# Optimization experiments

Hardware: AMD Instinct MI355X
Metric: run time of the kernel (lower is better)

## Reference

```python
import jax, jax.numpy as jnp
import numpy as np

# Dimensions
T, B = 128, 512
NTOK, NINP, NHID = 512, 512, 600
NB, BS, TOPK = 6, 100, 4          # num_blocks, block_size = nhid//num_blocks, update_topk
H, DK, DV, ATT = 4, 64, 85, 340   # input-attention heads, key dim, value dim (H*DV == attention_out)
H2, DK2, DV2 = 4, 32, 32          # communication (step) attention dims


def setup_inputs() -> dict:
    key = jax.random.key(0)
    ks = jax.random.split(key, 16)
    def rn(k, shape, s=0.05):
        return (jax.random.normal(k, shape) * s).astype(jnp.float32)
    return dict(
        input=jax.random.normal(ks[0], (T, B, NTOK), dtype=jnp.float32),
        h0=jnp.zeros((B, NHID), jnp.float32),
        masks=jnp.ones((T, B, 1), jnp.float32),
        enc_W=rn(ks[1], (NTOK, NINP)), enc_b=jnp.zeros((NINP,), jnp.float32),
        Wq_in=rn(ks[2], (BS, H * DK)), Wk_in=rn(ks[3], (NINP, H * DK)), Wv_in=rn(ks[4], (NINP, H * DV)),
        W_ih=rn(ks[5], (NB, ATT, 3 * BS)), W_hh=rn(ks[6], (NB, BS, 3 * BS)),
        b_ih=jnp.zeros((NB, 3 * BS), jnp.float32), b_hh=jnp.zeros((NB, 3 * BS), jnp.float32),
        Wq_c=rn(ks[7], (BS, H2 * DK2)), Wk_c=rn(ks[8], (BS, H2 * DK2)),
        Wv_c=rn(ks[9], (BS, H2 * DV2)), Wo_c=rn(ks[10], (H2 * DV2, BS)),
        dec_W=rn(ks[11], (NHID, NTOK)), dec_b=jnp.zeros((NTOK,), jnp.float32),
    )


def _rim_scan(emb, masks, h0, Wq_in, Wk_in, Wv_in, W_ih, W_hh, b_ih, b_hh,
              Wq_c, Wk_c, Wv_c, Wo_c):
    inv_sdk = 1.0 / np.sqrt(DK).astype(np.float32)
    inv_sdk2 = 1.0 / np.sqrt(DK2).astype(np.float32)

    def step(h, xm):
        xt, mt = xm                      # [B,NINP], [B,1]
        h = h * mt                       # episode-reset gating
        hb = h.reshape(B, NB, BS)
        # --- input attention over {real input, null} slots ---
        slots = jnp.stack([xt, jnp.zeros_like(xt)], axis=1)          # [B,2,NINP]
        k = (slots @ Wk_in).reshape(B, 2, H, DK)
        v = (slots @ Wv_in).reshape(B, 2, H, DV)
        q = (hb @ Wq_in).reshape(B, NB, H, DK)
        att = jax.nn.softmax(jnp.einsum('bnhd,bshd->bnhs', q, k) * inv_sdk, axis=-1)
        act = 1.0 - att[..., 1].mean(-1)                             # [B,NB] attention to real input
        kth = jax.lax.top_k(act, TOPK)[0][:, -1:]
        mask = (act >= kth).astype(h.dtype)                          # [B,NB] top-k block activation
        inp_use = jnp.einsum('bnhs,bshd->bnhd', att, v).reshape(B, NB, ATT)
        # --- block-diagonal GRU update ---
        gi = jnp.einsum('bnd,nde->bne', inp_use, W_ih) + b_ih
        gh = jnp.einsum('bnd,nde->bne', hb, W_hh) + b_hh
        gi_r, gi_z, gi_n = jnp.split(gi, 3, axis=-1)
        gh_r, gh_z, gh_n = jnp.split(gh, 3, axis=-1)
        r = jax.nn.sigmoid(gi_r + gh_r)
        z = jax.nn.sigmoid(gi_z + gh_z)
        n = jnp.tanh(gi_n + r * gh_n)
        hn = (1.0 - z) * n + z * hb
        # --- step (communication) attention across blocks, residual ---
        qc = (hn @ Wq_c).reshape(B, NB, H2, DK2)
        kc = (hn @ Wk_c).reshape(B, NB, H2, DK2)
        vc = (hn @ Wv_c).reshape(B, NB, H2, DV2)
        ac = jax.nn.softmax(jnp.einsum('bnhd,bmhd->bhnm', qc, kc) * inv_sdk2, axis=-1)
        co = jnp.einsum('bhnm,bmhd->bnhd', ac, vc).reshape(B, NB, H2 * DV2) @ Wo_c
        hc = hn + co
        # --- only top-k active blocks are updated ---
        m = mask[..., None]
        hf = (m * hc + (1.0 - m) * hb).reshape(B, NHID)
        return hf, (hf, mask)

    h_last, (hs, bmask) = jax.lax.scan(step, h0, (emb, masks))
    return hs, h_last, bmask


def reference(input, h0, masks, enc_W, enc_b, Wq_in, Wk_in, Wv_in,
              W_ih, W_hh, b_ih, b_hh, Wq_c, Wk_c, Wv_c, Wo_c, dec_W, dec_b):
    emb = input @ enc_W + enc_b                                      # encoder Linear [T,B,NINP]
    hs, h_last, bmask = _rim_scan(emb, masks, h0, Wq_in, Wk_in, Wv_in,
                                  W_ih, W_hh, b_ih, b_hh, Wq_c, Wk_c, Wv_c, Wo_c)
    dec = hs @ dec_W + dec_b                                         # decoder [T,B,NTOK]
    return dec
```

## Files before the change

### kernel.cpp

```cpp
#include <hip/hip_runtime.h>
#include <math.h>

#define T_STEPS 128
#define BATCH   512
#define NTOK    512
#define NINP    512
#define NHID    600
#define NBK     6
#define BS      100
#define HH      4
#define DK      64
#define DV      85
#define ATT     340
#define H2      4
#define DK2     32
#define DV2     32
#define G3      300
#define VN      340
#define KAPN    400
#define CN      740
#define CNP     768
#define UN2     1800
#define UN2P    1920
#define UK0     128
#define KV0     512
#define DECKP   640
#define SW      2

typedef __attribute__((ext_vector_type(8))) short short8;
typedef __attribute__((ext_vector_type(4))) float f32x4;

__device__ __forceinline__ float sigf(float x) { return 1.f / (1.f + expf(-x)); }
__device__ __forceinline__ unsigned short f2b(float f) {
    unsigned u = __float_as_uint(f);
    unsigned r = (u + 0x7fffu + ((u >> 16) & 1u)) >> 16;
    return (unsigned short)r;
}
__device__ __forceinline__ float b2f(unsigned short u) {
    return __uint_as_float(((unsigned)u) << 16);
}
__device__ __forceinline__ void split3(float x, unsigned short& hi,
                                       unsigned short& mid, unsigned short& lo) {
    hi = f2b(x);
    float r1 = x - b2f(hi);
    mid = f2b(r1);
    lo = f2b(r1 - b2f(mid));
}

struct ZOff { int div; long s1; long s2; };
__device__ __forceinline__ long zoff(ZOff z, int bz) {
    return (long)(bz / z.div) * z.s1 + (long)(bz % z.div) * z.s2;
}

__global__ __launch_bounds__(256) void gemm6(
    const unsigned short* __restrict__ A, long aZ, int aZdiv,
    const unsigned short* __restrict__ B, long bZ,
    float* __restrict__ C, long cZ, int ldc, int Nreal,
    const float* __restrict__ bias, int K0)
{
    const int bz = blockIdx.z;
    A += (long)(bz / aZdiv) * aZ;
    B += (long)bz * bZ;
    C += (long)bz * cZ;
    const int LDA = 3 * K0;
    const int m0 = blockIdx.y * 128, n0 = blockIdx.x * 128;
    __shared__ __align__(16) unsigned short As[128 * 64];
    __shared__ __align__(16) unsigned short Bs[128 * 64];
    const int tid = threadIdx.x;
    const int lane = tid & 63;
    const int wid = tid >> 6;
    const int wr = wid >> 1, wc = wid & 1;

    f32x4 acc[4][4];
#pragma unroll
    for (int m = 0; m < 4; m++)
#pragma unroll
        for (int n = 0; n < 4; n++)
#pragma unroll
            for (int v = 0; v < 4; v++) acc[m][n][v] = 0.f;

    const int segA[6] = {0, 0, 1, 0, 2, 1};
    const int segB[6] = {0, 1, 0, 2, 0, 1};
    for (int p = 0; p < 6; p++) {
        const unsigned short* Ap = A + segA[p] * K0;
        const unsigned short* Bp = B + segB[p] * K0;
        for (int k0 = 0; k0 < K0; k0 += 64) {
            short8 ra[4], rb[4];
#pragma unroll
            for (int q = 0; q < 4; q++) {
                int idx = (q << 8) + tid;
                int r = idx >> 3, ce = (idx & 7) << 3;
                ra[q] = *(const short8*)&Ap[(long)(m0 + r) * LDA + k0 + ce];
                rb[q] = *(const short8*)&Bp[(long)(n0 + r) * LDA + k0 + ce];
            }
            __syncthreads();
#pragma unroll
            for (int q = 0; q < 4; q++) {
                int idx = (q << 8) + tid;
                int r = idx >> 3, ce = (idx & 7) << 3;
                *(short8*)&As[r * 64 + ce] = ra[q];
                *(short8*)&Bs[r * 64 + ce] = rb[q];
            }
            __syncthreads();
#pragma unroll
            for (int kk = 0; kk < 2; kk++) {
                short8 af[4], bfr[4];
#pragma unroll
                for (int m = 0; m < 4; m++)
                    af[m] = *(const short8*)&As[(wr * 64 + m * 16 + (lane & 15)) * 64 + kk * 32 + (lane >> 4) * 8];
#pragma unroll
                for (int n = 0; n < 4; n++)
                    bfr[n] = *(const short8*)&Bs[(wc * 64 + n * 16 + (lane & 15)) * 64 + kk * 32 + (lane >> 4) * 8];
#pragma unroll
                for (int m = 0; m < 4; m++)
#pragma unroll
                    for (int n = 0; n < 4; n++)
                        acc[m][n] = __builtin_amdgcn_mfma_f32_16x16x32_bf16(af[m], bfr[n], acc[m][n], 0, 0, 0);
            }
        }
    }
#pragma unroll
    for (int m = 0; m < 4; m++) {
        int rbase = m0 + wr * 64 + m * 16 + (lane >> 4) * 4;
#pragma unroll
        for (int n = 0; n < 4; n++) {
            int col = n0 + wc * 64 + n * 16 + (lane & 15);
            if (col < Nreal) {
                float bv = bias ? bias[col] : 0.f;
#pragma unroll
                for (int v = 0; v < 4; v++)
                    C[(long)(rbase + v) * ldc + col] = acc[m][n][v] + bv;
            }
        }
    }
}

__global__ __launch_bounds__(256) void gemm6_kv(
    const unsigned short* __restrict__ A,
    const unsigned short* __restrict__ B,
    unsigned short* __restrict__ A_U,
    float* __restrict__ Kbuf,
    const float* __restrict__ bias, int K0, int MU)
{
    const int LDA = 3 * K0;
    const int m0 = blockIdx.y * 128, n0 = blockIdx.x * 128;
    __shared__ __align__(16) unsigned short As[128 * 64];
    __shared__ __align__(16) unsigned short Bs[128 * 64];
    const int tid = threadIdx.x;
    const int lane = tid & 63;
    const int wid = tid >> 6;
    const int wr = wid >> 1, wc = wid & 1;

    f32x4 acc[4][4];
#pragma unroll
    for (int m = 0; m < 4; m++)
#pragma unroll
        for (int n = 0; n < 4; n++)
#pragma unroll
            for (int v = 0; v < 4; v++) acc[m][n][v] = 0.f;

    const int segA[6] = {0, 0, 1, 0, 2, 1};
    const int segB[6] = {0, 1, 0, 2, 0, 1};
    for (int p = 0; p < 6; p++) {
        const unsigned short* Ap = A + segA[p] * K0;
        const unsigned short* Bp = B + segB[p] * K0;
        for (int k0 = 0; k0 < K0; k0 += 64) {
            short8 ra[4], rb[4];
#pragma unroll
            for (int q = 0; q < 4; q++) {
                int idx = (q << 8) + tid;
                int r = idx >> 3, ce = (idx & 7) << 3;
                ra[q] = *(const short8*)&Ap[(long)(m0 + r) * LDA + k0 + ce];
                rb[q] = *(const short8*)&Bp[(long)(n0 + r) * LDA + k0 + ce];
            }
            __syncthreads();
#pragma unroll
            for (int q = 0; q < 4; q++) {
                int idx = (q << 8) + tid;
                int r = idx >> 3, ce = (idx & 7) << 3;
                *(short8*)&As[r * 64 + ce] = ra[q];
                *(short8*)&Bs[r * 64 + ce] = rb[q];
            }
            __syncthreads();
#pragma unroll
            for (int kk = 0; kk < 2; kk++) {
                short8 af[4], bfr[4];
#pragma unroll
                for (int m = 0; m < 4; m++)
                    af[m] = *(const short8*)&As[(wr * 64 + m * 16 + (lane & 15)) * 64 + kk * 32 + (lane >> 4) * 8];
#pragma unroll
                for (int n = 0; n < 4; n++)
                    bfr[n] = *(const short8*)&Bs[(wc * 64 + n * 16 + (lane & 15)) * 64 + kk * 32 + (lane >> 4) * 8];
#pragma unroll
                for (int m = 0; m < 4; m++)
#pragma unroll
                    for (int n = 0; n < 4; n++)
                        acc[m][n] = __builtin_amdgcn_mfma_f32_16x16x32_bf16(af[m], bfr[n], acc[m][n], 0, 0, 0);
            }
        }
    }
#pragma unroll
    for (int m = 0; m < 4; m++) {
        int rbase = m0 + wr * 64 + m * 16 + (lane >> 4) * 4;
#pragma unroll
        for (int n = 0; n < 4; n++) {
            int col = n0 + wc * 64 + n * 16 + (lane & 15);
            if (col < CN) {
                float bv = bias[col];
                if (col < VN) {
                    int h = col / DV, kk2 = col - h * DV;
#pragma unroll
                    for (int v = 0; v < 4; v++) {
                        float val = acc[m][n][v] + bv;
                        unsigned short hi, mid, lo;
                        split3(val, hi, mid, lo);
                        long base = ((long)h * MU + (rbase + v)) * (3 * UK0) + kk2;
                        A_U[base] = hi;
                        A_U[base + UK0] = mid;
                        A_U[base + 2 * UK0] = lo;
                    }
                } else {
                    int kc = col - VN;
#pragma unroll
                    for (int v = 0; v < 4; v++)
                        Kbuf[(long)(rbase + v) * KAPN + kc] = acc[m][n][v] + bv;
                }
            }
        }
    }
}

__global__ __launch_bounds__(256) void gemm_mfma(
    const unsigned short* __restrict__ A,
    const unsigned short* __restrict__ B,
    float* __restrict__ C, int ldc,
    const float* __restrict__ bias, int Kp)
{
    const int m0 = blockIdx.y * 128, n0 = blockIdx.x * 128;
    __shared__ __align__(16) unsigned short As[128 * 64];
    __shared__ __align__(16) unsigned short Bs[128 * 64];
    const int tid = threadIdx.x;
    const int lane = tid & 63;
    const int wid = tid >> 6;
    const int wr = wid >> 1, wc = wid & 1;

    f32x4 acc[4][4];
#pragma unroll
    for (int m = 0; m < 4; m++)
#pragma unroll
        for (int n = 0; n < 4; n++)
#pragma unroll
            for (int v = 0; v < 4; v++) acc[m][n][v] = 0.f;

    for (int k0 = 0; k0 < Kp; k0 += 64) {
        short8 ra[4], rb[4];
#pragma unroll
        for (int q = 0; q < 4; q++) {
            int idx = (q << 8) + tid;
            int r = idx >> 3, ce = (idx & 7) << 3;
            ra[q] = *(const short8*)&A[(long)(m0 + r) * Kp + k0 + ce];
            rb[q] = *(const short8*)&B[(long)(n0 + r) * Kp + k0 + ce];
        }
        __syncthreads();
#pragma unroll
        for (int q = 0; q < 4; q++) {
            int idx = (q << 8) + tid;
            int r = idx >> 3, ce = (idx & 7) << 3;
            *(short8*)&As[r * 64 + ce] = ra[q];
            *(short8*)&Bs[r * 64 + ce] = rb[q];
        }
        __syncthreads();
#pragma unroll
        for (int kk = 0; kk < 2; kk++) {
            short8 af[4], bfr[4];
#pragma unroll
            for (int m = 0; m < 4; m++)
                af[m] = *(const short8*)&As[(wr * 64 + m * 16 + (lane & 15)) * 64 + kk * 32 + (lane >> 4) * 8];
#pragma unroll
            for (int n = 0; n < 4; n++)
                bfr[n] = *(const short8*)&Bs[(wc * 64 + n * 16 + (lane & 15)) * 64 + kk * 32 + (lane >> 4) * 8];
#pragma unroll
            for (int m = 0; m < 4; m++)
#pragma unroll
                for (int n = 0; n < 4; n++)
                    acc[m][n] = __builtin_amdgcn_mfma_f32_16x16x32_bf16(af[m], bfr[n], acc[m][n], 0, 0, 0);
        }
    }
#pragma unroll
    for (int m = 0; m < 4; m++) {
        int rbase = m0 + wr * 64 + m * 16 + (lane >> 4) * 4;
#pragma unroll
        for (int n = 0; n < 4; n++) {
            int col = n0 + wc * 64 + n * 16 + (lane & 15);
            float bv = bias ? bias[col] : 0.f;
#pragma unroll
            for (int v = 0; v < 4; v++)
                C[(long)(rbase + v) * ldc + col] = acc[m][n][v] + bv;
        }
    }
}

__global__ __launch_bounds__(256) void sgemm(
    const float* __restrict__ A, ZOff za, int lda,
    const float* __restrict__ B, ZOff zb, int ldb,
    float* __restrict__ C, ZOff zc, int ldc,
    int M, int N, int K)
{
    const int bz = blockIdx.z;
    A += zoff(za, bz);
    B += zoff(zb, bz);
    C += zoff(zc, bz);
    const int m0 = blockIdx.y * 128, n0 = blockIdx.x * 64;
    __shared__ float As[16][132];
    __shared__ float Bs[16][68];
    const int tid = threadIdx.x;
    const int tm = tid >> 4, tn = tid & 15;
    const int ar = tid >> 1, ak = (tid & 1) * 8;
    const int bk = tid >> 4, bn = (tid & 15) * 4;

    float acc[8][4];
#pragma unroll
    for (int i = 0; i < 8; i++)
#pragma unroll
        for (int j = 0; j < 4; j++) acc[i][j] = 0.f;

    for (int k0 = 0; k0 < K; k0 += 16) {
        float av[8], bv[4];
#pragma unroll
        for (int j = 0; j < 8; j++) {
            int gk = k0 + ak + j;
            av[j] = (gk < K) ? A[(long)(m0 + ar) * lda + gk] : 0.f;
        }
#pragma unroll
        for (int j = 0; j < 4; j++) {
            int gk = k0 + bk, gn = n0 + bn + j;
            bv[j] = (gk < K && gn < N) ? B[(long)gk * ldb + gn] : 0.f;
        }
        __syncthreads();
#pragma unroll
        for (int j = 0; j < 8; j++) As[ak + j][ar] = av[j];
#pragma unroll
        for (int j = 0; j < 4; j++) Bs[bk][bn + j] = bv[j];
        __syncthreads();
#pragma unroll
        for (int kk = 0; kk < 16; kk++) {
            float a[8], b[4];
#pragma unroll
            for (int i = 0; i < 8; i++) a[i] = As[kk][tm * 8 + i];
#pragma unroll
            for (int j = 0; j < 4; j++) b[j] = Bs[kk][tn * 4 + j];
#pragma unroll
            for (int i = 0; i < 8; i++)
#pragma unroll
                for (int j = 0; j < 4; j++)
                    acc[i][j] += a[i] * b[j];
        }
    }
#pragma unroll
    for (int i = 0; i < 8; i++) {
        int gm = m0 + tm * 8 + i;
#pragma unroll
        for (int j = 0; j < 4; j++) {
            int gn = n0 + tn * 4 + j;
            if (gn < N) C[(long)gm * ldc + gn] = acc[i][j];
        }
    }
}

__global__ __launch_bounds__(256) void prep_wqt(const float* __restrict__ Wq_in,
                                                float* __restrict__ WqT)
{
    int idx = blockIdx.x * 256 + threadIdx.x;
    if (idx >= HH * DK * BS) return;
    int h = idx / (DK * BS), r = idx - h * DK * BS, d = r / BS, w = r - d * BS;
    WqT[idx] = Wq_in[w * (HH * DK) + h * DK + d];
}

__global__ __launch_bounds__(256) void prep_whh4(const float* __restrict__ W_hh,
                                                 float* __restrict__ Whh4)
{
    int idx = blockIdx.x * 256 + threadIdx.x;
    if (idx >= NBK * BS * G3) return;
    int n = idx / (BS * G3), r = idx - n * (BS * G3);
    int d = r / G3, e = r - d * G3;
    int g = e / BS, w = e - g * BS;
    Whh4[(((long)n * BS + d) * BS + w) * 4 + g] = W_hh[idx];
}

__global__ __launch_bounds__(256) void bias_k(const float* __restrict__ enc_b,
                                              const float* __restrict__ Wk,
                                              float* __restrict__ kbf)
{
    int j = threadIdx.x;
    if (j >= HH * DK) return;
    float acc = 0.f;
    for (int d = 0; d < NINP; d++) acc += enc_b[d] * Wk[d * (HH * DK) + j];
    kbf[j] = acc;
}

__global__ __launch_bounds__(256) void bias_c_kernel(const float* __restrict__ enc_b,
                                                     const float* __restrict__ Wv,
                                                     const float* __restrict__ kbf,
                                                     const float* __restrict__ WqT,
                                                     float* __restrict__ bias_c)
{
    int j = blockIdx.x * 256 + threadIdx.x;
    if (j >= CNP) return;
    float acc = 0.f;
    if (j < VN) {
        for (int d = 0; d < NINP; d++) acc += enc_b[d] * Wv[d * (HH * DV) + j];
    } else if (j < CN) {
        int r = j - VN;
        int h = r / BS, w = r - h * BS;
        for (int d = 0; d < DK; d++)
            acc += kbf[h * DK + d] * WqT[(h * DK + d) * BS + w];
    }
    bias_c[j] = acc;
}

__global__ __launch_bounds__(256) void cvt_dec(const float* __restrict__ dec_W,
                                               unsigned short* __restrict__ dst)
{
    int idx = blockIdx.x * 256 + threadIdx.x;
    if (idx >= NTOK * DECKP) return;
    int n = idx / DECKP, k = idx - n * DECKP;
    dst[idx] = f2b(k < NHID ? dec_W[k * NTOK + n] : 0.f);
}

__global__ __launch_bounds__(256) void cvt_split_ew(const float* __restrict__ EWfull,
                                                    unsigned short* __restrict__ dst)
{
    int idx = blockIdx.x * 256 + threadIdx.x;
    if (idx >= CNP * NTOK) return;
    int n = idx / NTOK, k = idx - n * NTOK;
    float x = (n < CN) ? EWfull[(long)k * CNP + n] : 0.f;
    unsigned short hi, mid, lo;
    split3(x, hi, mid, lo);
    long base = (long)n * (3 * KV0) + k;
    dst[base] = hi;
    dst[base + KV0] = mid;
    dst[base + 2 * KV0] = lo;
}

__global__ __launch_bounds__(256) void cvt_split_bu2(const float* __restrict__ W_ih,
                                                     unsigned short* __restrict__ dst)
{
    int idx = blockIdx.x * 256 + threadIdx.x;
    if (idx >= HH * UN2P * UK0) return;
    int h = idx / (UN2P * UK0), r = idx - h * (UN2P * UK0);
    int j = r / UK0, kk = r - j * UK0;
    float x = 0.f;
    if (kk < DV && j < UN2) {
        int n = j / G3, e = j - n * G3;
        x = W_ih[((long)n * ATT + h * DV + kk) * G3 + e];
    }
    unsigned short hi, mid, lo;
    split3(x, hi, mid, lo);
    long base = ((long)h * UN2P + j) * (3 * UK0) + kk;
    dst[base] = hi;
    dst[base + UK0] = mid;
    dst[base + 2 * UK0] = lo;
}

__global__ __launch_bounds__(256) void cvt_split_in(const float* __restrict__ src,
                                                    unsigned short* __restrict__ dst, long rows)
{
    long total = rows * NTOK;
    long i = (long)blockIdx.x * 256 + threadIdx.x;
    long stride = (long)gridDim.x * 256;
    for (; i < total; i += stride) {
        long row = i / NTOK; int k = (int)(i - row * NTOK);
        unsigned short hi, mid, lo;
        split3(src[i], hi, mid, lo);
        long base = row * (3 * KV0) + k;
        dst[base] = hi;
        dst[base + KV0] = mid;
        dst[base + 2 * KV0] = lo;
    }
}

__global__ __launch_bounds__(1024) void step_fused(
    const float* __restrict__ h_prev,
    const float* __restrict__ masks_t,
    const float* __restrict__ Kbuf,
    const float* __restrict__ U,
    const float* __restrict__ b_ih, const float* __restrict__ b_hh,
    const float* __restrict__ Whh4,
    const float* __restrict__ Wq_c, const float* __restrict__ Wk_c,
    const float* __restrict__ Wv_c, const float* __restrict__ Wo_c,
    float* __restrict__ h_out,
    unsigned short* __restrict__ A_dec,
    int s_step, int MU)
{
    const int b0 = blockIdx.x * SW, tid = threadIdx.x;
    __shared__ __align__(16) float hbT[NHID][SW];
    __shared__ __align__(16) float hnT[NHID][SW];
    __shared__ __align__(16) float kp[SW][KAPN];
    __shared__ __align__(16) float qcb[SW][768], kcb[SW][768], vcb[SW][768];
    __shared__ __align__(16) float coT[NBK * 128][SW];
    __shared__ float part[SW * 96];
    __shared__ float att[SW][24], mk[SW][NBK];
    __shared__ float lg[SW][144];

    const long rowd0 = (long)s_step * BATCH + b0;
    const int n2 = (tid < 600) ? tid / 100 : 0;
    const int w2 = (tid < 600) ? tid - n2 * 100 : 0;

    float uraw[HH][3][SW];
    if (tid < 600) {
#pragma unroll
        for (int h = 0; h < HH; h++) {
            const float* Uh = U + ((long)h * MU + rowd0) * UN2 + n2 * G3;
#pragma unroll
            for (int s = 0; s < SW; s++)
#pragma unroll
                for (int g = 0; g < 3; g++)
                    uraw[h][g][s] = Uh[(long)s * UN2 + g * BS + w2];
        }
    }

    for (int i = tid; i < SW * NHID; i += 1024) {
        int s = i / NHID, j = i - s * NHID;
        hbT[j][s] = h_prev[(long)(b0 + s) * NHID + j] * masks_t[b0 + s];
    }
    for (int i = tid; i < SW * KAPN; i += 1024) {
        int s = i / KAPN, j = i - s * KAPN;
        kp[s][j] = Kbuf[(rowd0 + s) * KAPN + j];
    }
    __syncthreads();
    if (tid < SW * 96) {
        int g = tid >> 2, q = tid & 3;
        int s = g / 24, r = g - s * 24;
        int n = r >> 2, h = r & 3;
        float acc = 0.f;
        int w0 = q * 25;
        for (int w = w0; w < w0 + 25; w++) acc += hbT[n * BS + w][s] * kp[s][h * BS + w];
        part[tid] = acc;
    }
    __syncthreads();
    if (tid < SW * 24) {
        int s = tid / 24, r = tid - s * 24;
        float l = part[tid * 4] + part[tid * 4 + 1] + part[tid * 4 + 2] + part[tid * 4 + 3];
        att[s][r] = sigf(l * 0.125f);
    }
    __syncthreads();
    if (tid < SW) {
        float a[NBK], av[NBK];
        for (int n = 0; n < NBK; n++) {
            av[n] = 0.25f * (att[tid][n * 4] + att[tid][n * 4 + 1] + att[tid][n * 4 + 2] + att[tid][n * 4 + 3]);
            a[n] = av[n];
        }
        for (int i = 0; i < 4; i++) {
            int mx = i;
            for (int j = i + 1; j < NBK; j++) if (a[j] > a[mx]) mx = j;
            float t = a[i]; a[i] = a[mx]; a[mx] = t;
        }
        float kth = a[3];
        for (int n = 0; n < NBK; n++) mk[tid][n] = (av[n] >= kth) ? 1.f : 0.f;
    }

    if (tid < 600) {
        float gi[3][SW], gh[3][SW];
#pragma unroll
        for (int g = 0; g < 3; g++) {
            float bi = b_ih[n2 * G3 + g * BS + w2];
            float bh = b_hh[n2 * G3 + g * BS + w2];
#pragma unroll
            for (int s = 0; s < SW; s++) { gi[g][s] = bi; gh[g][s] = bh; }
        }
#pragma unroll
        for (int h = 0; h < HH; h++)
#pragma unroll
            for (int s = 0; s < SW; s++) {
                float a = att[s][n2 * 4 + h];
#pragma unroll
                for (int g = 0; g < 3; g++)
                    gi[g][s] += a * uraw[h][g][s];
            }
        const f32x4* Wn4 = ((const f32x4*)Whh4) + (long)n2 * BS * BS + w2;
#pragma unroll 10
        for (int d = 0; d < BS; d++) {
            f32x4 wv = Wn4[(long)d * BS];
            float2 hv = *(const float2*)&hbT[n2 * BS + d][0];
            gh[0][0] += wv[0] * hv.x; gh[0][1] += wv[0] * hv.y;
            gh[1][0] += wv[1] * hv.x; gh[1][1] += wv[1] * hv.y;
            gh[2][0] += wv[2] * hv.x; gh[2][1] += wv[2] * hv.y;
        }
        float2 hnv;
        {
            float rr0 = sigf(gi[0][0] + gh[0][0]);
            float zz0 = sigf(gi[1][0] + gh[1][0]);
            float ng0 = tanhf(gi[2][0] + rr0 * gh[2][0]);
            hnv.x = (1.f - zz0) * ng0 + zz0 * hbT[n2 * BS + w2][0];
            float rr1 = sigf(gi[0][1] + gh[0][1]);
            float zz1 = sigf(gi[1][1] + gh[1][1]);
            float ng1 = tanhf(gi[2][1] + rr1 * gh[2][1]);
            hnv.y = (1.f - zz1) * ng1 + zz1 * hbT[n2 * BS + w2][1];
        }
        *(float2*)&hnT[n2 * BS + w2][0] = hnv;
    }
    __syncthreads();

    if (tid < 768) {
        const int mat = tid >> 8, r = tid & 255, ng = r >> 7, c = r & 127;
        const float* W = (mat == 0) ? Wq_c : ((mat == 1) ? Wk_c : Wv_c);
        float acc[3][SW];
#pragma unroll
        for (int j = 0; j < 3; j++)
#pragma unroll
            for (int s = 0; s < SW; s++) acc[j][s] = 0.f;
#pragma unroll 10
        for (int d = 0; d < BS; d++) {
            float wv = W[d * 128 + c];
#pragma unroll
            for (int j = 0; j < 3; j++) {
                float2 hv = *(const float2*)&hnT[(ng * 3 + j) * BS + d][0];
                acc[j][0] += wv * hv.x;
                acc[j][1] += wv * hv.y;
            }
        }
        float (*dst)[768] = (mat == 0) ? qcb : ((mat == 1) ? kcb : vcb);
#pragma unroll
        for (int j = 0; j < 3; j++)
#pragma unroll
            for (int s = 0; s < SW; s++)
                dst[s][(ng * 3 + j) * 128 + c] = acc[j][s];
    }
    __syncthreads();

    if (tid < SW * 144) {
        int s = tid / 144, r = tid - s * 144;
        int h = r / 36, r2 = r - h * 36, n = r2 / NBK, m = r2 - n * NBK;
        float sv = 0.f;
#pragma unroll
        for (int e4 = 0; e4 < 8; e4++) {
            f32x4 qv = *(const f32x4*)&qcb[s][n * 128 + h * 32 + e4 * 4];
            f32x4 kv = *(const f32x4*)&kcb[s][m * 128 + h * 32 + e4 * 4];
            sv += qv[0] * kv[0] + qv[1] * kv[1] + qv[2] * kv[2] + qv[3] * kv[3];
        }
        lg[s][r] = sv * 0.17677669529663687f;
    }
    __syncthreads();
    if (tid < SW * 24) {
        int s = tid / 24, r = tid - s * 24;
        float* row = &lg[s][r * NBK];
        float mx = row[0];
        for (int m = 1; m < NBK; m++) mx = fmaxf(mx, row[m]);
        float sv = 0.f;
        for (int m = 0; m < NBK; m++) { row[m] = expf(row[m] - mx); sv += row[m]; }
        float inv = 1.f / sv;
        for (int m = 0; m < NBK; m++) row[m] *= inv;
    }
    __syncthreads();
    for (int idx = tid; idx < SW * 768; idx += 1024) {
        int s = idx / 768, r = idx - s * 768;
        int n = r >> 7, d = r & 127, h = d >> 5;
        float a = 0.f;
#pragma unroll
        for (int m = 0; m < NBK; m++) a += lg[s][h * 36 + n * NBK + m] * vcb[s][m * 128 + d];
        coT[r][s] = a;
    }
    __syncthreads();

    if (tid < 600) {
        float a0 = 0.f, a1 = 0.f;
#pragma unroll 8
        for (int d = 0; d < 128; d++) {
            float wv = Wo_c[d * BS + w2];
            float2 cv = *(const float2*)&coT[n2 * 128 + d][0];
            a0 += wv * cv.x;
            a1 += wv * cv.y;
        }
        float2 res;
        float hc0 = hnT[n2 * BS + w2][0] + a0;
        float hc1 = hnT[n2 * BS + w2][1] + a1;
        res.x = (mk[0][n2] > 0.5f) ? hc0 : hbT[n2 * BS + w2][0];
        res.y = (mk[1][n2] > 0.5f) ? hc1 : hbT[n2 * BS + w2][1];
        *(float2*)&hbT[n2 * BS + w2][0] = res;
    }
    __syncthreads();
    for (int i = tid; i < SW * NHID; i += 1024) {
        int s = i / NHID, j = i - s * NHID;
        h_out[(long)(b0 + s) * NHID + j] = hbT[j][s];
    }
    for (int i = tid; i < SW * DECKP; i += 1024) {
        int s = i / DECKP, col = i - s * DECKP;
        A_dec[(rowd0 + s) * DECKP + col] = f2b(col < NHID ? hbT[col][s] : 0.f);
    }
}

extern "C" void kernel_launch(void* const* d_in, const int* in_sizes, int n_in,
                              void* d_out, int out_size, void* d_ws, size_t ws_size,
                              hipStream_t stream)
{
    const float* input = (const float*)d_in[0];
    const float* h0    = (const float*)d_in[1];
    const float* masks = (const float*)d_in[2];
    const float* enc_W = (const float*)d_in[3];
    const float* enc_b = (const float*)d_in[4];
    const float* Wq_in = (const float*)d_in[5];
    const float* Wk_in = (const float*)d_in[6];
    const float* Wv_in = (const float*)d_in[7];
    const float* W_ih  = (const float*)d_in[8];
    const float* W_hh  = (const float*)d_in[9];
    const float* b_ih  = (const float*)d_in[10];
    const float* b_hh  = (const float*)d_in[11];
    const float* Wq_c  = (const float*)d_in[12];
    const float* Wk_c  = (const float*)d_in[13];
    const float* Wv_c  = (const float*)d_in[14];
    const float* Wo_c  = (const float*)d_in[15];
    const float* dec_W = (const float*)d_in[16];
    const float* dec_b = (const float*)d_in[17];
    float* out = (float*)d_out;

    const size_t AL = 256;
    auto pad = [&](size_t x) { return (x + AL - 1) & ~(AL - 1); };
    size_t fixedB = pad((size_t)NTOK * CNP * 4)
                  + pad((size_t)NTOK * 256 * 4)
                  + pad((size_t)HH * DK * BS * 4)
                  + pad((size_t)256 * 4)
                  + pad((size_t)CNP * 4)
                  + pad((size_t)NBK * BS * BS * 4 * 4)
                  + pad((size_t)CNP * 3 * KV0 * 2)
                  + pad((size_t)HH * UN2P * 3 * UK0 * 2)
                  + pad((size_t)NTOK * DECKP * 2)
                  + 2 * pad((size_t)BATCH * NHID * 4);
    auto perC = [&](int C) {
        size_t MU = (size_t)C * BATCH;
        return pad(MU * 3 * KV0 * 2)
             + pad(MU * KAPN * 4)
             + pad((size_t)HH * MU * 3 * UK0 * 2)
             + pad((size_t)HH * MU * UN2 * 4)
             + pad(MU * DECKP * 2);
    };
    int C = 8;
    while (C > 1 && fixedB + perC(C) > ws_size) C >>= 1;
    const int MU = C * BATCH;
    const int NCH = T_STEPS / C;

    char* p = (char*)d_ws;
    auto alloc = [&](size_t bytes) { char* r = p; p += pad(bytes); return r; };
    float*          EWfull = (float*)alloc((size_t)NTOK * CNP * 4);
    float*          EWk    = (float*)alloc((size_t)NTOK * 256 * 4);
    float*          WqT    = (float*)alloc((size_t)HH * DK * BS * 4);
    float*          kbf    = (float*)alloc((size_t)256 * 4);
    float*          bias_c = (float*)alloc((size_t)CNP * 4);
    float*          Whh4   = (float*)alloc((size_t)NBK * BS * BS * 4 * 4);
    unsigned short* B_vkap = (unsigned short*)alloc((size_t)CNP * 3 * KV0 * 2);
    unsigned short* B_U    = (unsigned short*)alloc((size_t)HH * UN2P * 3 * UK0 * 2);
    unsigned short* B_dec  = (unsigned short*)alloc((size_t)NTOK * DECKP * 2);
    float*          hA     = (float*)alloc((size_t)BATCH * NHID * 4);
    float*          hB     = (float*)alloc((size_t)BATCH * NHID * 4);
    unsigned short* A_in   = (unsigned short*)alloc((size_t)MU * 3 * KV0 * 2);
    float*          Kbuf   = (float*)alloc((size_t)MU * KAPN * 4);
    unsigned short* A_U    = (unsigned short*)alloc((size_t)HH * MU * 3 * UK0 * 2);
    float*          Ubuf   = (float*)alloc((size_t)HH * MU * UN2 * 4);
    unsigned short* A_dec  = (unsigned short*)alloc((size_t)MU * DECKP * 2);

    dim3 blk(256);
    ZOff z0 = {1, 0, 0};

    sgemm<<<dim3(6, 4, 1), blk, 0, stream>>>(
        enc_W, z0, NINP, Wv_in, z0, HH * DV, EWfull, z0, CNP, NTOK, VN, NINP);
    sgemm<<<dim3(4, 4, 1), blk, 0, stream>>>(
        enc_W, z0, NINP, Wk_in, z0, HH * DK, EWk, z0, 256, NTOK, HH * DK, NINP);
    prep_wqt<<<dim3((HH * DK * BS + 255) / 256), blk, 0, stream>>>(Wq_in, WqT);
    prep_whh4<<<dim3((NBK * BS * G3 + 255) / 256), blk, 0, stream>>>(W_hh, Whh4);
    sgemm<<<dim3(2, 4, HH), blk, 0, stream>>>(
        EWk, ZOff{1, DK, 0}, 256, WqT, ZOff{1, (long)DK * BS, 0}, BS,
        EWfull + VN, ZOff{1, BS, 0}, CNP, NTOK, BS, DK);
    bias_k<<<dim3(1), blk, 0, stream>>>(enc_b, Wk_in, kbf);
    bias_c_kernel<<<dim3(3), blk, 0, stream>>>(enc_b, Wv_in, kbf, WqT, bias_c);
    cvt_split_ew<<<dim3((CNP * NTOK + 255) / 256), blk, 0, stream>>>(EWfull, B_vkap);
    cvt_split_bu2<<<dim3((HH * UN2P * UK0 + 255) / 256), blk, 0, stream>>>(W_ih, B_U);
    cvt_dec<<<dim3((NTOK * DECKP + 255) / 256), blk, 0, stream>>>(dec_W, B_dec);

    const float* hp = h0;
    float* hbufs[2] = { hA, hB };
    int t = 0;
    for (int c = 0; c < NCH; c++) {
        cvt_split_in<<<dim3(2048), blk, 0, stream>>>(
            input + (size_t)c * MU * NTOK, A_in, MU);
        gemm6_kv<<<dim3(CNP / 128, MU / 128, 1), blk, 0, stream>>>(
            A_in, B_vkap, A_U, Kbuf, bias_c, KV0, MU);
        gemm6<<<dim3(UN2P / 128, MU / 128, HH), blk, 0, stream>>>(
            A_U, (long)MU * 3 * UK0, 1, B_U, (long)UN2P * 3 * UK0,
            Ubuf, (long)MU * UN2, UN2, UN2, nullptr, UK0);
        for (int s = 0; s < C; s++, t++) {
            float* hout = hbufs[t & 1];
            step_fused<<<dim3(BATCH / SW), dim3(1024), 0, stream>>>(
                hp, masks + (size_t)t * BATCH, Kbuf, Ubuf, b_ih, b_hh, Whh4,
                Wq_c, Wk_c, Wv_c, Wo_c, hout, A_dec, s, MU);
            hp = hout;
        }
        gemm_mfma<<<dim3(NTOK / 128, MU / 128, 1), blk, 0, stream>>>(
            A_dec, B_dec, out + (size_t)c * MU * NTOK, NTOK, dec_b, DECKP);
    }
}
```

Before: 6.374 ms.

## Fuse per-step recurrent kernels into one chunk kernel; stage GEMM tiles via global_load_lds

```diff
diff --git a/kernel.cpp b/kernel.cpp
--- a/kernel.cpp
+++ b/kernel.cpp
@@ -30,6 +30,9 @@
 typedef __attribute__((ext_vector_type(8))) short short8;
 typedef __attribute__((ext_vector_type(4))) float f32x4;
 
+typedef __attribute__((address_space(1))) const unsigned int* g1ptr;
+typedef __attribute__((address_space(3))) unsigned int* l3ptr;
+
 __device__ __forceinline__ float sigf(float x) { return 1.f / (1.f + expf(-x)); }
 __device__ __forceinline__ unsigned short f2b(float f) {
     unsigned u = __float_as_uint(f);
@@ -50,6 +53,21 @@
 struct ZOff { int div; long s1; long s2; };
 __device__ __forceinline__ long zoff(ZOff z, int bz) {
     return (long)(bz / z.div) * z.s1 + (long)(bz % z.div) * z.s2;
+}
+
+__device__ __forceinline__ void stage_tile(const unsigned short* __restrict__ gbase,
+                                           long rowStride, int m0, int k0,
+                                           unsigned short* lds, int tid)
+{
+    const int w = tid >> 6;
+#pragma unroll
+    for (int q = 0; q < 4; q++) {
+        int idx = (q << 8) + tid;
+        int r = idx >> 3, ce = (idx & 7) << 3;
+        const unsigned short* g = gbase + (long)(m0 + r) * rowStride + k0 + ce;
+        unsigned short* l = lds + q * 2048 + w * 512;
+        __builtin_amdgcn_global_load_lds((g1ptr)(const void*)g, (l3ptr)(void*)l, 16, 0, 0);
+    }
 }
 
 __global__ __launch_bounds__(256) void gemm6(
@@ -85,22 +103,9 @@
         const unsigned short* Ap = A + segA[p] * K0;
         const unsigned short* Bp = B + segB[p] * K0;
         for (int k0 = 0; k0 < K0; k0 += 64) {
-            short8 ra[4], rb[4];
-#pragma unroll
-            for (int q = 0; q < 4; q++) {
-                int idx = (q << 8) + tid;
-                int r = idx >> 3, ce = (idx & 7) << 3;
-                ra[q] = *(const short8*)&Ap[(long)(m0 + r) * LDA + k0 + ce];
-                rb[q] = *(const short8*)&Bp[(long)(n0 + r) * LDA + k0 + ce];
-            }
             __syncthreads();
-#pragma unroll
-            for (int q = 0; q < 4; q++) {
-                int idx = (q << 8) + tid;
-                int r = idx >> 3, ce = (idx & 7) << 3;
-                *(short8*)&As[r * 64 + ce] = ra[q];
-                *(short8*)&Bs[r * 64 + ce] = rb[q];
-            }
+            stage_tile(Ap, LDA, m0, k0, As, tid);
+            stage_tile(Bp, LDA, n0, k0, Bs, tid);
             __syncthreads();
 #pragma unroll
             for (int kk = 0; kk < 2; kk++) {
@@ -165,22 +170,9 @@
         const unsigned short* Ap = A + segA[p] * K0;
         const unsigned short* Bp = B + segB[p] * K0;
         for (int k0 = 0; k0 < K0; k0 += 64) {
-            short8 ra[4], rb[4];
-#pragma unroll
-            for (int q = 0; q < 4; q++) {
-                int idx = (q << 8) + tid;
-                int r = idx >> 3, ce = (idx & 7) << 3;
-                ra[q] = *(const short8*)&Ap[(long)(m0 + r) * LDA + k0 + ce];
-                rb[q] = *(const short8*)&Bp[(long)(n0 + r) * LDA + k0 + ce];
-            }
             __syncthreads();
-#pragma unroll
-            for (int q = 0; q < 4; q++) {
-                int idx = (q << 8) + tid;
-                int r = idx >> 3, ce = (idx & 7) << 3;
-                *(short8*)&As[r * 64 + ce] = ra[q];
-                *(short8*)&Bs[r * 64 + ce] = rb[q];
-            }
+            stage_tile(Ap, LDA, m0, k0, As, tid);
+            stage_tile(Bp, LDA, n0, k0, Bs, tid);
             __syncthreads();
 #pragma unroll
             for (int kk = 0; kk < 2; kk++) {
@@ -253,22 +245,9 @@
             for (int v = 0; v < 4; v++) acc[m][n][v] = 0.f;
 
     for (int k0 = 0; k0 < Kp; k0 += 64) {
-        short8 ra[4], rb[4];
-#pragma unroll
-        for (int q = 0; q < 4; q++) {
-            int idx = (q << 8) + tid;
-            int r = idx >> 3, ce = (idx & 7) << 3;
-            ra[q] = *(const short8*)&A[(long)(m0 + r) * Kp + k0 + ce];
-            rb[q] = *(const short8*)&B[(long)(n0 + r) * Kp + k0 + ce];
-        }
-        __syncthreads();
-#pragma unroll
-        for (int q = 0; q < 4; q++) {
-            int idx = (q << 8) + tid;
-            int r = idx >> 3, ce = (idx & 7) << 3;
-            *(short8*)&As[r * 64 + ce] = ra[q];
-            *(short8*)&Bs[r * 64 + ce] = rb[q];
-        }
+        __syncthreads();
+        stage_tile(A, Kp, m0, k0, As, tid);
+        stage_tile(B, Kp, n0, k0, Bs, tid);
         __syncthreads();
 #pragma unroll
         for (int kk = 0; kk < 2; kk++) {
@@ -479,18 +458,18 @@
     }
 }
 
-__global__ __launch_bounds__(1024) void step_fused(
-    const float* __restrict__ h_prev,
-    const float* __restrict__ masks_t,
+__global__ __launch_bounds__(1024) void step_chunk(
+    const float* __restrict__ h_in,
+    const float* __restrict__ masks_c,
     const float* __restrict__ Kbuf,
     const float* __restrict__ U,
     const float* __restrict__ b_ih, const float* __restrict__ b_hh,
     const float* __restrict__ Whh4,
     const float* __restrict__ Wq_c, const float* __restrict__ Wk_c,
     const float* __restrict__ Wv_c, const float* __restrict__ Wo_c,
-    float* __restrict__ h_out,
+    float* __restrict__ h_outG,
     unsigned short* __restrict__ A_dec,
-    int s_step, int MU)
+    int nsteps, int MU)
 {
     const int b0 = blockIdx.x * SW, tid = threadIdx.x;
     __shared__ __align__(16) float hbT[NHID][SW];
@@ -502,190 +481,198 @@
     __shared__ float att[SW][24], mk[SW][NBK];
     __shared__ float lg[SW][144];
 
-    const long rowd0 = (long)s_step * BATCH + b0;
     const int n2 = (tid < 600) ? tid / 100 : 0;
     const int w2 = (tid < 600) ? tid - n2 * 100 : 0;
 
-    float uraw[HH][3][SW];
-    if (tid < 600) {
-#pragma unroll
-        for (int h = 0; h < HH; h++) {
-            const float* Uh = U + ((long)h * MU + rowd0) * UN2 + n2 * G3;
-#pragma unroll
-            for (int s = 0; s < SW; s++)
-#pragma unroll
-                for (int g = 0; g < 3; g++)
-                    uraw[h][g][s] = Uh[(long)s * UN2 + g * BS + w2];
-        }
-    }
-
     for (int i = tid; i < SW * NHID; i += 1024) {
         int s = i / NHID, j = i - s * NHID;
-        hbT[j][s] = h_prev[(long)(b0 + s) * NHID + j] * masks_t[b0 + s];
-    }
-    for (int i = tid; i < SW * KAPN; i += 1024) {
-        int s = i / KAPN, j = i - s * KAPN;
-        kp[s][j] = Kbuf[(rowd0 + s) * KAPN + j];
-    }
-    __syncthreads();
-    if (tid < SW * 96) {
-        int g = tid >> 2, q = tid & 3;
-        int s = g / 24, r = g - s * 24;
-        int n = r >> 2, h = r & 3;
-        float acc = 0.f;
-        int w0 = q * 25;
-        for (int w = w0; w < w0 + 25; w++) acc += hbT[n * BS + w][s] * kp[s][h * BS + w];
-        part[tid] = acc;
-    }
-    __syncthreads();
-    if (tid < SW * 24) {
-        int s = tid / 24, r = tid - s * 24;
-        float l = part[tid * 4] + part[tid * 4 + 1] + part[tid * 4 + 2] + part[tid * 4 + 3];
-        att[s][r] = sigf(l * 0.125f);
-    }
-    __syncthreads();
-    if (tid < SW) {
-        float a[NBK], av[NBK];
-        for (int n = 0; n < NBK; n++) {
-            av[n] = 0.25f * (att[tid][n * 4] + att[tid][n * 4 + 1] + att[tid][n * 4 + 2] + att[tid][n * 4 + 3]);
-            a[n] = av[n];
-        }
-        for (int i = 0; i < 4; i++) {
-            int mx = i;
-            for (int j = i + 1; j < NBK; j++) if (a[j] > a[mx]) mx = j;
-            float t = a[i]; a[i] = a[mx]; a[mx] = t;
-        }
-        float kth = a[3];
-        for (int n = 0; n < NBK; n++) mk[tid][n] = (av[n] >= kth) ? 1.f : 0.f;
-    }
-
-    if (tid < 600) {
-        float gi[3][SW], gh[3][SW];
-#pragma unroll
-        for (int g = 0; g < 3; g++) {
-            float bi = b_ih[n2 * G3 + g * BS + w2];
-            float bh = b_hh[n2 * G3 + g * BS + w2];
-#pragma unroll
-            for (int s = 0; s < SW; s++) { gi[g][s] = bi; gh[g][s] = bh; }
-        }
-#pragma unroll
-        for (int h = 0; h < HH; h++)
-#pragma unroll
-            for (int s = 0; s < SW; s++) {
-                float a = att[s][n2 * 4 + h];
-#pragma unroll
-                for (int g = 0; g < 3; g++)
-                    gi[g][s] += a * uraw[h][g][s];
-            }
-        const f32x4* Wn4 = ((const f32x4*)Whh4) + (long)n2 * BS * BS + w2;
+        hbT[j][s] = h_in[(long)(b0 + s) * NHID + j];
+    }
+
+    for (int st = 0; st < nsteps; st++) {
+        const long rowd0 = (long)st * BATCH + b0;
+
+        float uraw[HH][3][SW];
+        if (tid < 600) {
+#pragma unroll
+            for (int h = 0; h < HH; h++) {
+                const float* Uh = U + ((long)h * MU + rowd0) * UN2 + n2 * G3;
+#pragma unroll
+                for (int s = 0; s < SW; s++)
+#pragma unroll
+                    for (int g = 0; g < 3; g++)
+                        uraw[h][g][s] = Uh[(long)s * UN2 + g * BS + w2];
+            }
+        }
+        __syncthreads();
+        for (int i = tid; i < SW * NHID; i += 1024) {
+            int s = i / NHID, j = i - s * NHID;
+            hbT[j][s] *= masks_c[rowd0 + s];
+        }
+        for (int i = tid; i < SW * KAPN; i += 1024) {
+            int s = i / KAPN, j = i - s * KAPN;
+            kp[s][j] = Kbuf[(rowd0 + s) * KAPN + j];
+        }
+        __syncthreads();
+        if (tid < SW * 96) {
+            int g = tid >> 2, q = tid & 3;
+            int s = g / 24, r = g - s * 24;
+            int n = r >> 2, h = r & 3;
+            float acc = 0.f;
+            int w0 = q * 25;
+            for (int w = w0; w < w0 + 25; w++) acc += hbT[n * BS + w][s] * kp[s][h * BS + w];
+            part[tid] = acc;
+        }
+        __syncthreads();
+        if (tid < SW * 24) {
+            int s = tid / 24, r = tid - s * 24;
+            float l = part[tid * 4] + part[tid * 4 + 1] + part[tid * 4 + 2] + part[tid * 4 + 3];
+            att[s][r] = sigf(l * 0.125f);
+        }
+        __syncthreads();
+        if (tid < SW) {
+            float a[NBK], av[NBK];
+            for (int n = 0; n < NBK; n++) {
+                av[n] = 0.25f * (att[tid][n * 4] + att[tid][n * 4 + 1] + att[tid][n * 4 + 2] + att[tid][n * 4 + 3]);
+                a[n] = av[n];
+            }
+            for (int i = 0; i < 4; i++) {
+                int mx = i;
+                for (int j = i + 1; j < NBK; j++) if (a[j] > a[mx]) mx = j;
+                float t = a[i]; a[i] = a[mx]; a[mx] = t;
+            }
+            float kth = a[3];
+            for (int n = 0; n < NBK; n++) mk[tid][n] = (av[n] >= kth) ? 1.f : 0.f;
+        }
+
+        if (tid < 600) {
+            float gi[3][SW], gh[3][SW];
+#pragma unroll
+            for (int g = 0; g < 3; g++) {
+                float bi = b_ih[n2 * G3 + g * BS + w2];
+                float bh = b_hh[n2 * G3 + g * BS + w2];
+#pragma unroll
+                for (int s = 0; s < SW; s++) { gi[g][s] = bi; gh[g][s] = bh; }
+            }
+#pragma unroll
+            for (int h = 0; h < HH; h++)
+#pragma unroll
+                for (int s = 0; s < SW; s++) {
+                    float a = att[s][n2 * 4 + h];
+#pragma unroll
+                    for (int g = 0; g < 3; g++)
+                        gi[g][s] += a * uraw[h][g][s];
+                }
+            const f32x4* Wn4 = ((const f32x4*)Whh4) + (long)n2 * BS * BS + w2;
 #pragma unroll 10
-        for (int d = 0; d < BS; d++) {
-            f32x4 wv = Wn4[(long)d * BS];
-            float2 hv = *(const float2*)&hbT[n2 * BS + d][0];
-            gh[0][0] += wv[0] * hv.x; gh[0][1] += wv[0] * hv.y;
-            gh[1][0] += wv[1] * hv.x; gh[1][1] += wv[1] * hv.y;
-            gh[2][0] += wv[2] * hv.x; gh[2][1] += wv[2] * hv.y;
-        }
-        float2 hnv;
-        {
-            float rr0 = sigf(gi[0][0] + gh[0][0]);
-            float zz0 = sigf(gi[1][0] + gh[1][0]);
-            float ng0 = tanhf(gi[2][0] + rr0 * gh[2][0]);
-            hnv.x = (1.f - zz0) * ng0 + zz0 * hbT[n2 * BS + w2][0];
-            float rr1 = sigf(gi[0][1] + gh[0][1]);
-            float zz1 = sigf(gi[1][1] + gh[1][1]);
-            float ng1 = tanhf(gi[2][1] + rr1 * gh[2][1]);
-            hnv.y = (1.f - zz1) * ng1 + zz1 * hbT[n2 * BS + w2][1];
-        }
-        *(float2*)&hnT[n2 * BS + w2][0] = hnv;
-    }
-    __syncthreads();
-
-    if (tid < 768) {
-        const int mat = tid >> 8, r = tid & 255, ng = r >> 7, c = r & 127;
-        const float* W = (mat == 0) ? Wq_c : ((mat == 1) ? Wk_c : Wv_c);
-        float acc[3][SW];
-#pragma unroll
-        for (int j = 0; j < 3; j++)
-#pragma unroll
-            for (int s = 0; s < SW; s++) acc[j][s] = 0.f;
+            for (int d = 0; d < BS; d++) {
+                f32x4 wv = Wn4[(long)d * BS];
+                float2 hv = *(const float2*)&hbT[n2 * BS + d][0];
+                gh[0][0] += wv[0] * hv.x; gh[0][1] += wv[0] * hv.y;
+                gh[1][0] += wv[1] * hv.x; gh[1][1] += wv[1] * hv.y;
+                gh[2][0] += wv[2] * hv.x; gh[2][1] += wv[2] * hv.y;
+            }
+            float2 hnv;
+            {
+                float rr0 = sigf(gi[0][0] + gh[0][0]);
+                float zz0 = sigf(gi[1][0] + gh[1][0]);
+                float ng0 = tanhf(gi[2][0] + rr0 * gh[2][0]);
+                hnv.x = (1.f - zz0) * ng0 + zz0 * hbT[n2 * BS + w2][0];
+                float rr1 = sigf(gi[0][1] + gh[0][1]);
+                float zz1 = sigf(gi[1][1] + gh[1][1]);
+                float ng1 = tanhf(gi[2][1] + rr1 * gh[2][1]);
+                hnv.y = (1.f - zz1) * ng1 + zz1 * hbT[n2 * BS + w2][1];
+            }
+            *(float2*)&hnT[n2 * BS + w2][0] = hnv;
+        }
+        __syncthreads();
+
+        if (tid < 768) {
+            const int mat = tid >> 8, r = tid & 255, ng = r >> 7, c = r & 127;
+            const float* W = (mat == 0) ? Wq_c : ((mat == 1) ? Wk_c : Wv_c);
+            float acc[3][SW];
+#pragma unroll
+            for (int j = 0; j < 3; j++)
+#pragma unroll
+                for (int s = 0; s < SW; s++) acc[j][s] = 0.f;
 #pragma unroll 10
-        for (int d = 0; d < BS; d++) {
-            float wv = W[d * 128 + c];
-#pragma unroll
-            for (int j = 0; j < 3; j++) {
-                float2 hv = *(const float2*)&hnT[(ng * 3 + j) * BS + d][0];
-                acc[j][0] += wv * hv.x;
-                acc[j][1] += wv * hv.y;
-            }
-        }
-        float (*dst)[768] = (mat == 0) ? qcb : ((mat == 1) ? kcb : vcb);
-#pragma unroll
-        for (int j = 0; j < 3; j++)
-#pragma unroll
-            for (int s = 0; s < SW; s++)
-                dst[s][(ng * 3 + j) * 128 + c] = acc[j][s];
-    }
-    __syncthreads();
-
-    if (tid < SW * 144) {
-        int s = tid / 144, r = tid - s * 144;
-        int h = r / 36, r2 = r - h * 36, n = r2 / NBK, m = r2 - n * NBK;
-        float sv = 0.f;
-#pragma unroll
-        for (int e4 = 0; e4 < 8; e4++) {
-            f32x4 qv = *(const f32x4*)&qcb[s][n * 128 + h * 32 + e4 * 4];
-            f32x4 kv = *(const f32x4*)&kcb[s][m * 128 + h * 32 + e4 * 4];
-            sv += qv[0] * kv[0] + qv[1] * kv[1] + qv[2] * kv[2] + qv[3] * kv[3];
-        }
-        lg[s][r] = sv * 0.17677669529663687f;
-    }
-    __syncthreads();
-    if (tid < SW * 24) {
-        int s = tid / 24, r = tid - s * 24;
-        float* row = &lg[s][r * NBK];
-        float mx = row[0];
-        for (int m = 1; m < NBK; m++) mx = fmaxf(mx, row[m]);
-        float sv = 0.f;
-        for (int m = 0; m < NBK; m++) { row[m] = expf(row[m] - mx); sv += row[m]; }
-        float inv = 1.f / sv;
-        for (int m = 0; m < NBK; m++) row[m] *= inv;
-    }
-    __syncthreads();
-    for (int idx = tid; idx < SW * 768; idx += 1024) {
-        int s = idx / 768, r = idx - s * 768;
-        int n = r >> 7, d = r & 127, h = d >> 5;
-        float a = 0.f;
-#pragma unroll
-        for (int m = 0; m < NBK; m++) a += lg[s][h * 36 + n * NBK + m] * vcb[s][m * 128 + d];
-        coT[r][s] = a;
-    }
-    __syncthreads();
-
-    if (tid < 600) {
-        float a0 = 0.f, a1 = 0.f;
+            for (int d = 0; d < BS; d++) {
+                float wv = W[d * 128 + c];
+#pragma unroll
+                for (int j = 0; j < 3; j++) {
+                    float2 hv = *(const float2*)&hnT[(ng * 3 + j) * BS + d][0];
+                    acc[j][0] += wv * hv.x;
+                    acc[j][1] += wv * hv.y;
+                }
+            }
+            float (*dst)[768] = (mat == 0) ? qcb : ((mat == 1) ? kcb : vcb);
+#pragma unroll
+            for (int j = 0; j < 3; j++)
+#pragma unroll
+                for (int s = 0; s < SW; s++)
+                    dst[s][(ng * 3 + j) * 128 + c] = acc[j][s];
+        }
+        __syncthreads();
+
+        if (tid < SW * 144) {
+            int s = tid / 144, r = tid - s * 144;
+            int h = r / 36, r2 = r - h * 36, n = r2 / NBK, m = r2 - n * NBK;
+            float sv = 0.f;
+#pragma unroll
+            for (int e4 = 0; e4 < 8; e4++) {
+                f32x4 qv = *(const f32x4*)&qcb[s][n * 128 + h * 32 + e4 * 4];
+                f32x4 kv = *(const f32x4*)&kcb[s][m * 128 + h * 32 + e4 * 4];
+                sv += qv[0] * kv[0] + qv[1] * kv[1] + qv[2] * kv[2] + qv[3] * kv[3];
+            }
+            lg[s][r] = sv * 0.17677669529663687f;
+        }
+        __syncthreads();
+        if (tid < SW * 24) {
+            int s = tid / 24, r = tid - s * 24;
+            float* row = &lg[s][r * NBK];
+            float mx = row[0];
+            for (int m = 1; m < NBK; m++) mx = fmaxf(mx, row[m]);
+            float sv = 0.f;
+            for (int m = 0; m < NBK; m++) { row[m] = expf(row[m] - mx); sv += row[m]; }
+            float inv = 1.f / sv;
+            for (int m = 0; m < NBK; m++) row[m] *= inv;
+        }
+        __syncthreads();
+        for (int idx = tid; idx < SW * 768; idx += 1024) {
+            int s = idx / 768, r = idx - s * 768;
+            int n = r >> 7, d = r & 127, h = d >> 5;
+            float a = 0.f;
+#pragma unroll
+            for (int m = 0; m < NBK; m++) a += lg[s][h * 36 + n * NBK + m] * vcb[s][m * 128 + d];
+            coT[r][s] = a;
+        }
+        __syncthreads();
+
+        if (tid < 600) {
+            float a0 = 0.f, a1 = 0.f;
 #pragma unroll 8
-        for (int d = 0; d < 128; d++) {
-            float wv = Wo_c[d * BS + w2];
-            float2 cv = *(const float2*)&coT[n2 * 128 + d][0];
-            a0 += wv * cv.x;
-            a1 += wv * cv.y;
-        }
-        float2 res;
-        float hc0 = hnT[n2 * BS + w2][0] + a0;
-        float hc1 = hnT[n2 * BS + w2][1] + a1;
-        res.x = (mk[0][n2] > 0.5f) ? hc0 : hbT[n2 * BS + w2][0];
-        res.y = (mk[1][n2] > 0.5f) ? hc1 : hbT[n2 * BS + w2][1];
-        *(float2*)&hbT[n2 * BS + w2][0] = res;
-    }
-    __syncthreads();
+            for (int d = 0; d < 128; d++) {
+                float wv = Wo_c[d * BS + w2];
+                float2 cv = *(const float2*)&coT[n2 * 128 + d][0];
+                a0 += wv * cv.x;
+                a1 += wv * cv.y;
+            }
+            float2 res;
+            float hc0 = hnT[n2 * BS + w2][0] + a0;
+            float hc1 = hnT[n2 * BS + w2][1] + a1;
+            res.x = (mk[0][n2] > 0.5f) ? hc0 : hbT[n2 * BS + w2][0];
+            res.y = (mk[1][n2] > 0.5f) ? hc1 : hbT[n2 * BS + w2][1];
+            *(float2*)&hbT[n2 * BS + w2][0] = res;
+        }
+        __syncthreads();
+        for (int i = tid; i < SW * DECKP; i += 1024) {
+            int s = i / DECKP, col = i - s * DECKP;
+            A_dec[(rowd0 + s) * DECKP + col] = f2b(col < NHID ? hbT[col][s] : 0.f);
+        }
+    }
     for (int i = tid; i < SW * NHID; i += 1024) {
         int s = i / NHID, j = i - s * NHID;
-        h_out[(long)(b0 + s) * NHID + j] = hbT[j][s];
-    }
-    for (int i = tid; i < SW * DECKP; i += 1024) {
-        int s = i / DECKP, col = i - s * DECKP;
-        A_dec[(rowd0 + s) * DECKP + col] = f2b(col < NHID ? hbT[col][s] : 0.f);
+        h_outG[(long)(b0 + s) * NHID + j] = hbT[j][s];
     }
 }
 
@@ -724,7 +711,7 @@
                   + pad((size_t)CNP * 3 * KV0 * 2)
                   + pad((size_t)HH * UN2P * 3 * UK0 * 2)
                   + pad((size_t)NTOK * DECKP * 2)
-                  + 2 * pad((size_t)BATCH * NHID * 4);
+                  + pad((size_t)BATCH * NHID * 4);
     auto perC = [&](int C) {
         size_t MU = (size_t)C * BATCH;
         return pad(MU * 3 * KV0 * 2)
@@ -750,7 +737,6 @@
     unsigned short* B_U    = (unsigned short*)alloc((size_t)HH * UN2P * 3 * UK0 * 2);
     unsigned short* B_dec  = (unsigned short*)alloc((size_t)NTOK * DECKP * 2);
     float*          hA     = (float*)alloc((size_t)BATCH * NHID * 4);
-    float*          hB     = (float*)alloc((size_t)BATCH * NHID * 4);
     unsigned short* A_in   = (unsigned short*)alloc((size_t)MU * 3 * KV0 * 2);
     float*          Kbuf   = (float*)alloc((size_t)MU * KAPN * 4);
     unsigned short* A_U    = (unsigned short*)alloc((size_t)HH * MU * 3 * UK0 * 2);
@@ -776,8 +762,6 @@
     cvt_dec<<<dim3((NTOK * DECKP + 255) / 256), blk, 0, stream>>>(dec_W, B_dec);
 
     const float* hp = h0;
-    float* hbufs[2] = { hA, hB };
-    int t = 0;
     for (int c = 0; c < NCH; c++) {
         cvt_split_in<<<dim3(2048), blk, 0, stream>>>(
             input + (size_t)c * MU * NTOK, A_in, MU);
@@ -786,13 +770,10 @@
         gemm6<<<dim3(UN2P / 128, MU / 128, HH), blk, 0, stream>>>(
             A_U, (long)MU * 3 * UK0, 1, B_U, (long)UN2P * 3 * UK0,
             Ubuf, (long)MU * UN2, UN2, UN2, nullptr, UK0);
-        for (int s = 0; s < C; s++, t++) {
-            float* hout = hbufs[t & 1];
-            step_fused<<<dim3(BATCH / SW), dim3(1024), 0, stream>>>(
-                hp, masks + (size_t)t * BATCH, Kbuf, Ubuf, b_ih, b_hh, Whh4,
-                Wq_c, Wk_c, Wv_c, Wo_c, hout, A_dec, s, MU);
-            hp = hout;
-        }
+        step_chunk<<<dim3(BATCH / SW), dim3(1024), 0, stream>>>(
+            hp, masks + (size_t)c * C * BATCH, Kbuf, Ubuf, b_ih, b_hh, Whh4,
+            Wq_c, Wk_c, Wv_c, Wo_c, hA, A_dec, C, MU);
+        hp = hA;
         gemm_mfma<<<dim3(NTOK / 128, MU / 128, 1), blk, 0, stream>>>(
             A_dec, B_dec, out + (size_t)c * MU * NTOK, NTOK, dec_b, DECKP);
     }
```

New measurement: 8.009 ms. +25.6%, slower.
